# Optimization experiments

Hardware: AMD Instinct MI355X
Metric: run time of the kernel (lower is better)

The kernel has to match this reference:

```python
import jax, jax.numpy as jnp
import numpy as np

N_NODES = 100000
N_EDGES = 3200000
N_PAIRS = 500000
D_IN = 256
D_HID = 256
D_OUT = 2


def setup_inputs() -> dict:
    key = jax.random.key(0)
    ks = jax.random.split(key, 9)
    s1 = 1.0 / np.sqrt(D_IN)
    s2 = 1.0 / np.sqrt(D_HID)
    s3 = 1.0 / np.sqrt(2 * D_HID)
    return {
        "x": jax.random.normal(ks[0], (N_NODES, D_IN), jnp.float32),
        "edge_index": jax.random.randint(ks[1], (2, N_EDGES), 0, N_NODES, jnp.int64 if jax.config.jax_enable_x64 else jnp.int32),
        "index": jax.random.randint(ks[2], (N_PAIRS, 2), 0, N_NODES, jnp.int64 if jax.config.jax_enable_x64 else jnp.int32),
        "W1": jax.random.normal(ks[3], (D_HID, D_IN), jnp.float32) * s1,
        "b1": jnp.zeros((D_HID,), jnp.float32),
        "W2": jax.random.normal(ks[4], (D_HID, D_HID), jnp.float32) * s2,
        "b2": jnp.zeros((D_HID,), jnp.float32),
        "W3": jax.random.normal(ks[5], (D_OUT, 2 * D_HID), jnp.float32) * s3,
        "b3": jnp.zeros((D_OUT,), jnp.float32),
    }


def _gin_conv(x, edge_index, W, b):
    # PyG GINConv (eps=0): nn((1+eps)*x + sum_{j in N(i)} x_j)
    src, dst = edge_index[0], edge_index[1]
    agg = jax.ops.segment_sum(x[src], dst, num_segments=x.shape[0])  # [N, d]
    return (x + agg) @ W.T + b


def reference(x, edge_index, index, W1, b1, W2, b2, W3, b3):
    h = jax.nn.relu(_gin_conv(x, edge_index, W1, b1))   # [N, D_HID]
    h = jax.nn.relu(_gin_conv(h, edge_index, W2, b2))   # [N, D_HID]
    pair = jnp.concatenate((h[index[:, 0]], h[index[:, 1]]), axis=-1)  # [P, 2*D_HID]
    logits = pair @ W3.T + b3                            # [P, D_OUT]
    return jax.nn.log_softmax(logits, axis=1)
```

## Files before the change

### kernel.cpp

```cpp
#include <hip/hip_runtime.h>
#include <hip/hip_bf16.h>

constexpr int N_NODES = 100000;
constexpr int N_EDGES = 3200000;
constexpr int N_PAIRS = 500000;
constexpr int D       = 256;
constexpr int NRANGE  = 8;
constexpr int RSPAN   = 12500;
constexpr int SCANN   = 100352;
constexpr int RCAP    = 410000;

using frag_ab = __attribute__((ext_vector_type(8))) short;
using frag_cd = __attribute__((ext_vector_type(4))) float;
typedef unsigned short ushort8 __attribute__((ext_vector_type(8)));

static __device__ __forceinline__ float b2f(unsigned short u) {
  return __uint_as_float(((unsigned)u) << 16);
}
static __device__ __forceinline__ unsigned short f2bf(float f) {
  unsigned u = __float_as_uint(f);
  unsigned r = (u + 0x7fff + ((u >> 16) & 1)) >> 16;
  return (unsigned short)r;
}

__global__ void conv_all(const float4* __restrict__ x, const float4* __restrict__ W1,
                         const float4* __restrict__ W2, ushort4* __restrict__ xb,
                         ushort4* __restrict__ W1b, ushort4* __restrict__ W2b,
                         int4* __restrict__ counts4, int* __restrict__ rc, int n4x) {
  const int nconv = n4x + 2 * 16384;
  const int total = nconv + SCANN / 4;
  int i = blockIdx.x * blockDim.x + threadIdx.x;
  if (i < NRANGE) rc[i] = i * RCAP;
  const int stride = gridDim.x * blockDim.x;
  for (; i < total; i += stride) {
    if (i < nconv) {
      float4 v; ushort4* dst; int k;
      if (i < n4x) { v = x[i]; dst = xb; k = i; }
      else if (i < n4x + 16384) { k = i - n4x; v = W1[k]; dst = W1b; }
      else { k = i - n4x - 16384; v = W2[k]; dst = W2b; }
      ushort4 o;
      o.x = f2bf(v.x); o.y = f2bf(v.y); o.z = f2bf(v.z); o.w = f2bf(v.w);
      dst[k] = o;
    } else {
      int4 z; z.x = 0; z.y = 0; z.z = 0; z.w = 0;
      counts4[i - nconv] = z;
    }
  }
}

constexpr int PART_SEG = 4096;
__global__ __launch_bounds__(256) void part_hist(const int* __restrict__ ei,
                                                 int* __restrict__ counts,
                                                 int* __restrict__ rc,
                                                 int* __restrict__ bucket) {
  __shared__ int lcnt[NRANGE];
  __shared__ int lbase[NRANGE];
  const int t = threadIdx.x;
  const int base = blockIdx.x * PART_SEG;
  if (t < NRANGE) lcnt[t] = 0;
  __syncthreads();

  int rnk[16], rng[16], pv[16];
#pragma unroll
  for (int j = 0; j < 16; ++j) {
    const int i = base + j * 256 + t;
    if (i < N_EDGES) {
      const int sv = ei[i];
      const int dv = ei[N_EDGES + i];
      atomicAdd(&counts[dv], 1);
      rng[j] = dv / RSPAN;
      pv[j] = sv | ((dv - rng[j] * RSPAN) << 17);
      rnk[j] = atomicAdd(&lcnt[rng[j]], 1);
    } else rng[j] = -1;
  }
  __syncthreads();
  if (t < NRANGE) lbase[t] = atomicAdd(&rc[t], lcnt[t]);
  __syncthreads();
#pragma unroll
  for (int j = 0; j < 16; ++j) {
    if (rng[j] >= 0) bucket[lbase[rng[j]] + rnk[j]] = pv[j];
  }
}

__global__ __launch_bounds__(1024) void scan_block_k(const int* __restrict__ in,
                                                     int* __restrict__ out,
                                                     int* __restrict__ bsum) {
  __shared__ int wsum[16];
  const int t = threadIdx.x, lane = t & 63, w = t >> 6;
  const int gid = blockIdx.x * 1024 + t;
  const int v = in[gid];
  int s = v;
#pragma unroll
  for (int off = 1; off < 64; off <<= 1) {
    int u = __shfl_up(s, off, 64);
    if (lane >= off) s += u;
  }
  if (lane == 63) wsum[w] = s;
  __syncthreads();
  if (t < 16) {
    int ws = wsum[t];
#pragma unroll
    for (int off = 1; off < 16; off <<= 1) {
      int u = __shfl_up(ws, off, 64);
      if (lane >= off) ws += u;
    }
    wsum[t] = ws;
  }
  __syncthreads();
  const int wpre = (w == 0) ? 0 : wsum[w - 1];
  out[gid] = wpre + s - v;
  if (t == 1023) bsum[blockIdx.x] = wsum[15];
}

__global__ __launch_bounds__(1024) void scan_small(const int* __restrict__ in,
                                                   int* __restrict__ out, int n) {
  __shared__ int wsum[16];
  const int t = threadIdx.x, lane = t & 63, w = t >> 6;
  int v = (t < n) ? in[t] : 0;
  int s = v;
#pragma unroll
  for (int off = 1; off < 64; off <<= 1) {
    int u = __shfl_up(s, off, 64);
    if (lane >= off) s += u;
  }
  if (lane == 63) wsum[w] = s;
  __syncthreads();
  if (t < 16) {
    int ws = wsum[t];
#pragma unroll
    for (int off = 1; off < 16; off <<= 1) {
      int u = __shfl_up(ws, off, 64);
      if (lane >= off) ws += u;
    }
    wsum[t] = ws;
  }
  __syncthreads();
  const int wpre = (w == 0) ? 0 : wsum[w - 1];
  if (t < n) out[t] = wpre + s - v;
}

__global__ __launch_bounds__(1024) void scan_add_k(int* __restrict__ cursor,
                                                   int* __restrict__ pos,
                                                   const int* __restrict__ bsum2) {
  const int gid = blockIdx.x * 1024 + threadIdx.x;
  const int v = cursor[gid] + bsum2[gid >> 10];
  cursor[gid] = v;
  pos[gid] = v;
}

constexpr int FLB = 128;
__global__ __launch_bounds__(256) void fill_local(const int* __restrict__ bucket,
                                                  const int* __restrict__ rc,
                                                  int* __restrict__ pos,
                                                  int* __restrict__ csr) {
  const int r = blockIdx.x & 7;
  const int j = blockIdx.x >> 3;
  const int rbase = r * RSPAN;
  const int beg = r * RCAP;
  const int end = rc[r];
  for (int i = beg + j * 256 + threadIdx.x; i < end; i += FLB * 256) {
    const int e = bucket[i];
    const int src = e & 0x1FFFF;
    const int dst = rbase + (e >> 17);
    const int p = atomicAdd(&pos[dst], 1);
    csr[p] = src;
  }
}

__global__ __launch_bounds__(256) void gather_agg_bf16(const ushort* __restrict__ x,
                                                       const int* __restrict__ csr,
                                                       const int* __restrict__ cursor,
                                                       const int* __restrict__ counts,
                                                       ushort* __restrict__ out) {
  const int node = blockIdx.x * 4 + (threadIdx.x >> 6);
  const int lane = threadIdx.x & 63;
  const int half = lane >> 5;
  const int fl   = lane & 31;
  if (node >= N_NODES) return;
  const int beg = cursor[node];
  const int end = beg + counts[node];
  const size_t fo = (size_t)fl * 8;

  float acc[8];
#pragma unroll
  for (int j = 0; j < 8; ++j) acc[j] = 0.f;

  if (half == 0) {
    const ushort8 self = *reinterpret_cast<const ushort8*>(x + (size_t)node * D + fo);
#pragma unroll
    for (int j = 0; j < 8; ++j) acc[j] += b2f(self[j]);
  }

  int o = beg + half;
  for (; o + 6 < end; o += 8) {
    const int s0 = csr[o], s1 = csr[o + 2], s2 = csr[o + 4], s3 = csr[o + 6];
    const ushort8 v0 = *reinterpret_cast<const ushort8*>(x + (size_t)s0 * D + fo);
    const ushort8 v1 = *reinterpret_cast<const ushort8*>(x + (size_t)s1 * D + fo);
    const ushort8 v2 = *reinterpret_cast<const ushort8*>(x + (size_t)s2 * D + fo);
    const ushort8 v3 = *reinterpret_cast<const ushort8*>(x + (size_t)s3 * D + fo);
#pragma unroll
    for (int j = 0; j < 8; ++j)
      acc[j] += (b2f(v0[j]) + b2f(v1[j])) + (b2f(v2[j]) + b2f(v3[j]));
  }
  for (; o < end; o += 2) {
    const ushort8 v = *reinterpret_cast<const ushort8*>(x + (size_t)csr[o] * D + fo);
#pragma unroll
    for (int j = 0; j < 8; ++j) acc[j] += b2f(v[j]);
  }

#pragma unroll
  for (int j = 0; j < 8; ++j) acc[j] += __shfl_xor(acc[j], 32, 64);

  if (half == 0) {
    ushort8 ov;
#pragma unroll
    for (int j = 0; j < 8; ++j) ov[j] = f2bf(acc[j]);
    *reinterpret_cast<ushort8*>(out + (size_t)node * D + fo) = ov;
  }
}

constexpr int GEMM_NWG = ((N_NODES + 63) / 64) * 4;
constexpr int GEMM_Q   = GEMM_NWG / 8;
constexpr int GEMM_R   = GEMM_NWG % 8;
constexpr int CT_PITCH = 72;

template <bool WRITE_C>
__global__ __launch_bounds__(256) void gemm_mfma(const ushort* __restrict__ A,
                                                 const ushort* __restrict__ W,
                                                 const float* __restrict__ bias,
                                                 ushort* __restrict__ C,
                                                 const float* __restrict__ W3,
                                                 float* __restrict__ projp,
                                                 int M) {
  __shared__ __align__(16) ushort As[64 * 256];
  __shared__ __align__(16) ushort Ws[64 * 256];

  const int orig = blockIdx.x;
  const int xcd  = orig & 7;
  const int jj   = orig >> 3;
  const int base_ = (xcd < GEMM_R) ? xcd * (GEMM_Q + 1)
                                   : GEMM_R * (GEMM_Q + 1) + (xcd - GEMM_R) * GEMM_Q;
  const int swz  = base_ + jj;
  const int row0 = (swz >> 2) * 64;
  const int col0 = (swz & 3) * 64;
  const int ct   = swz & 3;

  const int t = threadIdx.x;
  const int w = t >> 6, l = t & 63;

  {
    const float4 zero4 = {0.f, 0.f, 0.f, 0.f};
#pragma unroll
    for (int i = 0; i < 8; ++i) {
      const int chunk = t + i * 256;
      const int r  = chunk >> 5;
      const int kb = (chunk & 31) << 4;
      const int swzb = kb ^ ((r & 7) << 4);
      const int grow = row0 + r;
      float4 av = zero4;
      if (grow < M)
        av = *reinterpret_cast<const float4*>(
            reinterpret_cast<const char*>(A) + (size_t)grow * 512 + kb);
      *reinterpret_cast<float4*>(reinterpret_cast<char*>(As) + r * 512 + swzb) = av;
      const float4 wv = *reinterpret_cast<const float4*>(
          reinterpret_cast<const char*>(W) + (size_t)(col0 + r) * 512 + kb);
      *reinterpret_cast<float4*>(reinterpret_cast<char*>(Ws) + r * 512 + swzb) = wv;
    }
  }
  __syncthreads();

  const int g  = l >> 4;
  const int fr = l & 15;

  frag_cd acc[4];
#pragma unroll
  for (int c = 0; c < 4; ++c) {
    acc[c][0] = 0.f; acc[c][1] = 0.f; acc[c][2] = 0.f; acc[c][3] = 0.f;
  }

  const int arow = w * 16 + fr;
  const char* Asb = reinterpret_cast<const char*>(As);
  const char* Wsb = reinterpret_cast<const char*>(Ws);
#pragma unroll
  for (int ks = 0; ks < 8; ++ks) {
    const int kb = ks * 64 + g * 16;
    const frag_ab af = *reinterpret_cast<const frag_ab*>(
        Asb + arow * 512 + (kb ^ ((arow & 7) << 4)));
#pragma unroll
    for (int c = 0; c < 4; ++c) {
      const int wrow = c * 16 + fr;
      const frag_ab bf = *reinterpret_cast<const frag_ab*>(
          Wsb + wrow * 512 + (kb ^ ((wrow & 7) << 4)));
      acc[c] = __builtin_amdgcn_mfma_f32_16x16x32_bf16(af, bf, acc[c], 0, 0, 0);
    }
  }
  __syncthreads();

  ushort* Ct = As;
#pragma unroll
  for (int c = 0; c < 4; ++c) {
    const int col = c * 16 + fr;
    const float bv = bias[col0 + col];
#pragma unroll
    for (int r = 0; r < 4; ++r) {
      const int rl = w * 16 + g * 4 + r;
      Ct[rl * CT_PITCH + col] = f2bf(fmaxf(acc[c][r] + bv, 0.f));
    }
  }
  __syncthreads();

  if constexpr (WRITE_C) {
#pragma unroll
    for (int i = 0; i < 2; ++i) {
      const int chunk = t + i * 256;
      const int r  = chunk >> 3;
      const int cb = (chunk & 7) << 4;
      const int grow = row0 + r;
      if (grow < M)
        *reinterpret_cast<float4*>(reinterpret_cast<char*>(C) + (size_t)grow * 512 + col0 * 2 + cb) =
            *reinterpret_cast<const float4*>(
                reinterpret_cast<const char*>(Ct) + r * (CT_PITCH * 2) + cb);
    }
  } else {
    const int r = t >> 2;
    const int q = t & 3;
    const int grow = row0 + r;
    float pa0 = 0.f, pa1 = 0.f, pb0 = 0.f, pb1 = 0.f;
    if (grow < M) {
      const ushort8 u8a = *reinterpret_cast<const ushort8*>(&Ct[r * CT_PITCH + q * 16]);
      const ushort8 u8b = *reinterpret_cast<const ushort8*>(&Ct[r * CT_PITCH + q * 16 + 8]);
#pragma unroll
      for (int j = 0; j < 16; ++j) {
        const float hv = b2f(j < 8 ? u8a[j] : u8b[j - 8]);
        const int gc = col0 + q * 16 + j;
        pa0 += hv * W3[gc];
        pa1 += hv * W3[512 + gc];
        pb0 += hv * W3[256 + gc];
        pb1 += hv * W3[768 + gc];
      }
    }
    pa0 += __shfl_xor(pa0, 1, 64); pa0 += __shfl_xor(pa0, 2, 64);
    pa1 += __shfl_xor(pa1, 1, 64); pa1 += __shfl_xor(pa1, 2, 64);
    pb0 += __shfl_xor(pb0, 1, 64); pb0 += __shfl_xor(pb0, 2, 64);
    pb1 += __shfl_xor(pb1, 1, 64); pb1 += __shfl_xor(pb1, 2, 64);
    if (q == 0 && grow < M) {
      float4 o; o.x = pa0; o.y = pa1; o.z = pb0; o.w = pb1;
      *reinterpret_cast<float4*>(&projp[((size_t)ct * N_NODES + grow) * 4]) = o;
    }
  }
}

__global__ __launch_bounds__(256) void proj_reduce(const float4* __restrict__ projp,
                                                   float4* __restrict__ proj) {
  const int node = blockIdx.x * blockDim.x + threadIdx.x;
  if (node >= N_NODES) return;
  float4 s = projp[node];
#pragma unroll
  for (int ct = 1; ct < 4; ++ct) {
    const float4 v = projp[(size_t)ct * N_NODES + node];
    s.x += v.x; s.y += v.y; s.z += v.z; s.w += v.w;
  }
  proj[node] = s;
}

__global__ __launch_bounds__(256) void pair_lite(const float4* __restrict__ proj,
                                                 const int* __restrict__ idx,
                                                 const float* __restrict__ b3,
                                                 float* __restrict__ out) {
  const int p = blockIdx.x * blockDim.x + threadIdx.x;
  if (p >= N_PAIRS) return;
  const int2 ii = reinterpret_cast<const int2*>(idx)[p];
  const float4 pa = proj[ii.x];
  const float4 pb = proj[ii.y];
  float l0 = pa.x + pb.z + b3[0];
  float l1 = pa.y + pb.w + b3[1];
  const float m = fmaxf(l0, l1);
  const float lse = m + logf(expf(l0 - m) + expf(l1 - m));
  float2 o; o.x = l0 - lse; o.y = l1 - lse;
  reinterpret_cast<float2*>(out)[p] = o;
}

extern "C" void kernel_launch(void* const* d_in, const int* in_sizes, int n_in,
                              void* d_out, int out_size, void* d_ws, size_t ws_size,
                              hipStream_t stream) {
  const float* x   = (const float*)d_in[0];
  const int*   ei  = (const int*)d_in[1];
  const int*   idx = (const int*)d_in[2];
  const float* W1  = (const float*)d_in[3];
  const float* b1  = (const float*)d_in[4];
  const float* W2  = (const float*)d_in[5];
  const float* b2  = (const float*)d_in[6];
  const float* W3  = (const float*)d_in[7];
  const float* b3  = (const float*)d_in[8];
  float* out = (float*)d_out;

  char* ws = (char*)d_ws;
  ushort* xb    = (ushort*)(ws);
  ushort* aggb  = (ushort*)(ws + 51200000);
  int*    bucket= (int*)(ws + 51200000);
  ushort* hb    = (ushort*)(ws + 102400000);
  float* projp  = (float*)(ws + 102400000);
  float* projf  = (float*)(ws + 108800000);
  ushort* W1b   = (ushort*)(ws + 153600000);
  ushort* W2b   = (ushort*)(ws + 153731072);
  int* counts   = (int*)(ws + 153862144);
  int* cursor   = (int*)(ws + 154263552);
  int* pos      = (int*)(ws + 154664960);
  int* csr      = (int*)(ws + 155066368);
  int* bsum     = (int*)(ws + 169466368);
  int* bsum2    = (int*)(ws + 169466880);
  int* rc       = (int*)(ws + 169467392);

  const dim3 blk(256);
  const size_t feat = (size_t)N_NODES * D;
  constexpr int SCAN_BLOCKS = SCANN / 1024;
  const dim3 partGrid((N_EDGES + PART_SEG - 1) / PART_SEG);
  const dim3 flocGrid(NRANGE * FLB);
  const dim3 nodeGrid((N_NODES + 3) / 4);
  const dim3 gemmGrid(GEMM_NWG);
  const dim3 nodeThreadGrid((N_NODES + 255) / 256);
  const dim3 pairGrid((N_PAIRS + 255) / 256);

  conv_all<<<dim3(4096), blk, 0, stream>>>((const float4*)x, (const float4*)W1,
                                           (const float4*)W2, (ushort4*)xb,
                                           (ushort4*)W1b, (ushort4*)W2b,
                                           (int4*)counts, rc, (int)(feat / 4));

  part_hist<<<partGrid, blk, 0, stream>>>(ei, counts, rc, bucket);
  scan_block_k<<<dim3(SCAN_BLOCKS), dim3(1024), 0, stream>>>(counts, cursor, bsum);
  scan_small<<<1, 1024, 0, stream>>>(bsum, bsum2, SCAN_BLOCKS);
  scan_add_k<<<dim3(SCAN_BLOCKS), dim3(1024), 0, stream>>>(cursor, pos, bsum2);
  fill_local<<<flocGrid, blk, 0, stream>>>(bucket, rc, pos, csr);

  gather_agg_bf16<<<nodeGrid, blk, 0, stream>>>(xb, csr, cursor, counts, aggb);
  gemm_mfma<true><<<gemmGrid, blk, 0, stream>>>(aggb, W1b, b1, hb, nullptr, nullptr, N_NODES);

  gather_agg_bf16<<<nodeGrid, blk, 0, stream>>>(hb, csr, cursor, counts, aggb);
  gemm_mfma<false><<<gemmGrid, blk, 0, stream>>>(aggb, W2b, b2, nullptr, W3, projp, N_NODES);

  proj_reduce<<<nodeThreadGrid, blk, 0, stream>>>((const float4*)projp, (float4*)projf);
  pair_lite<<<pairGrid, blk, 0, stream>>>((const float4*)projf, idx, b3, out);
}
```

Baseline: 897.1 us.

## Fuse conversion with partitioning, merge scan passes, drop pos array and proj_reduce

Edge partitioning now shares a kernel with the bf16 conversion of features and weights, so the two run concurrently in one launch; zeroing moves to memsets. The three-stage scan becomes two kernels, with each block re-summing the block totals serially. fill_local takes slots by decrementing counts instead of using a separate pos array, and gather reads cursor[node+1] for the end. proj_reduce is folded into the pair kernel, which now reads four partial projections per endpoint. This cuts launches and memory passes, but doubles random gathers in the pair stage and adds a serial loop per scan block.

```diff
diff --git a/kernel.cpp b/kernel.cpp
--- a/kernel.cpp
+++ b/kernel.cpp
@@ -23,17 +23,53 @@
   return (unsigned short)r;
 }
 
-__global__ void conv_all(const float4* __restrict__ x, const float4* __restrict__ W1,
-                         const float4* __restrict__ W2, ushort4* __restrict__ xb,
-                         ushort4* __restrict__ W1b, ushort4* __restrict__ W2b,
-                         int4* __restrict__ counts4, int* __restrict__ rc, int n4x) {
-  const int nconv = n4x + 2 * 16384;
-  const int total = nconv + SCANN / 4;
-  int i = blockIdx.x * blockDim.x + threadIdx.x;
-  if (i < NRANGE) rc[i] = i * RCAP;
-  const int stride = gridDim.x * blockDim.x;
-  for (; i < total; i += stride) {
-    if (i < nconv) {
+constexpr int PART_SEG    = 4096;
+constexpr int PART_BLOCKS = (N_EDGES + PART_SEG - 1) / PART_SEG;
+constexpr int CONV_BLOCKS = 4096;
+
+__global__ __launch_bounds__(256) void conv_part(const int* __restrict__ ei,
+                                                 int* __restrict__ counts,
+                                                 int* __restrict__ rc,
+                                                 int* __restrict__ bucket,
+                                                 const float4* __restrict__ x,
+                                                 const float4* __restrict__ W1,
+                                                 const float4* __restrict__ W2,
+                                                 ushort4* __restrict__ xb,
+                                                 ushort4* __restrict__ W1b,
+                                                 ushort4* __restrict__ W2b, int n4x) {
+  const int t = threadIdx.x;
+  if (blockIdx.x < PART_BLOCKS) {
+    __shared__ int lcnt[NRANGE];
+    __shared__ int lbase[NRANGE];
+    const int base = blockIdx.x * PART_SEG;
+    if (t < NRANGE) lcnt[t] = 0;
+    __syncthreads();
+
+    int rnk[16], rng[16], pv[16];
+#pragma unroll
+    for (int j = 0; j < 16; ++j) {
+      const int i = base + j * 256 + t;
+      if (i < N_EDGES) {
+        const int sv = ei[i];
+        const int dv = ei[N_EDGES + i];
+        atomicAdd(&counts[dv], 1);
+        rng[j] = dv / RSPAN;
+        pv[j] = sv | ((dv - rng[j] * RSPAN) << 17);
+        rnk[j] = atomicAdd(&lcnt[rng[j]], 1);
+      } else rng[j] = -1;
+    }
+    __syncthreads();
+    if (t < NRANGE) lbase[t] = t * RCAP + atomicAdd(&rc[t], lcnt[t]);
+    __syncthreads();
+#pragma unroll
+    for (int j = 0; j < 16; ++j) {
+      if (rng[j] >= 0) bucket[lbase[rng[j]] + rnk[j]] = pv[j];
+    }
+  } else {
+    const int nconv = n4x + 2 * 16384;
+    int i = (blockIdx.x - PART_BLOCKS) * 256 + t;
+    const int stride = CONV_BLOCKS * 256;
+    for (; i < nconv; i += stride) {
       float4 v; ushort4* dst; int k;
       if (i < n4x) { v = x[i]; dst = xb; k = i; }
       else if (i < n4x + 16384) { k = i - n4x; v = W1[k]; dst = W1b; }
@@ -41,44 +77,7 @@
       ushort4 o;
       o.x = f2bf(v.x); o.y = f2bf(v.y); o.z = f2bf(v.z); o.w = f2bf(v.w);
       dst[k] = o;
-    } else {
-      int4 z; z.x = 0; z.y = 0; z.z = 0; z.w = 0;
-      counts4[i - nconv] = z;
-    }
-  }
-}
-
-constexpr int PART_SEG = 4096;
-__global__ __launch_bounds__(256) void part_hist(const int* __restrict__ ei,
-                                                 int* __restrict__ counts,
-                                                 int* __restrict__ rc,
-                                                 int* __restrict__ bucket) {
-  __shared__ int lcnt[NRANGE];
-  __shared__ int lbase[NRANGE];
-  const int t = threadIdx.x;
-  const int base = blockIdx.x * PART_SEG;
-  if (t < NRANGE) lcnt[t] = 0;
-  __syncthreads();
-
-  int rnk[16], rng[16], pv[16];
-#pragma unroll
-  for (int j = 0; j < 16; ++j) {
-    const int i = base + j * 256 + t;
-    if (i < N_EDGES) {
-      const int sv = ei[i];
-      const int dv = ei[N_EDGES + i];
-      atomicAdd(&counts[dv], 1);
-      rng[j] = dv / RSPAN;
-      pv[j] = sv | ((dv - rng[j] * RSPAN) << 17);
-      rnk[j] = atomicAdd(&lcnt[rng[j]], 1);
-    } else rng[j] = -1;
-  }
-  __syncthreads();
-  if (t < NRANGE) lbase[t] = atomicAdd(&rc[t], lcnt[t]);
-  __syncthreads();
-#pragma unroll
-  for (int j = 0; j < 16; ++j) {
-    if (rng[j] >= 0) bucket[lbase[rng[j]] + rnk[j]] = pv[j];
+    }
   }
 }
 
@@ -112,57 +111,40 @@
   if (t == 1023) bsum[blockIdx.x] = wsum[15];
 }
 
-__global__ __launch_bounds__(1024) void scan_small(const int* __restrict__ in,
-                                                   int* __restrict__ out, int n) {
-  __shared__ int wsum[16];
-  const int t = threadIdx.x, lane = t & 63, w = t >> 6;
-  int v = (t < n) ? in[t] : 0;
-  int s = v;
-#pragma unroll
-  for (int off = 1; off < 64; off <<= 1) {
-    int u = __shfl_up(s, off, 64);
-    if (lane >= off) s += u;
-  }
-  if (lane == 63) wsum[w] = s;
-  __syncthreads();
-  if (t < 16) {
-    int ws = wsum[t];
-#pragma unroll
-    for (int off = 1; off < 16; off <<= 1) {
-      int u = __shfl_up(ws, off, 64);
-      if (lane >= off) ws += u;
-    }
-    wsum[t] = ws;
-  }
-  __syncthreads();
-  const int wpre = (w == 0) ? 0 : wsum[w - 1];
-  if (t < n) out[t] = wpre + s - v;
-}
-
-__global__ __launch_bounds__(1024) void scan_add_k(int* __restrict__ cursor,
-                                                   int* __restrict__ pos,
-                                                   const int* __restrict__ bsum2) {
-  const int gid = blockIdx.x * 1024 + threadIdx.x;
-  const int v = cursor[gid] + bsum2[gid >> 10];
-  cursor[gid] = v;
-  pos[gid] = v;
+constexpr int SCAN_BLOCKS = SCANN / 1024;
+__global__ __launch_bounds__(1024) void scan_addf(int* __restrict__ cursor,
+                                                  const int* __restrict__ bsum) {
+  __shared__ int bs[SCAN_BLOCKS];
+  __shared__ int bs2[SCAN_BLOCKS];
+  const int t = threadIdx.x;
+  if (t < SCAN_BLOCKS) bs[t] = bsum[t];
+  __syncthreads();
+  if (t == 0) {
+    int run = 0;
+#pragma unroll 1
+    for (int k = 0; k < SCAN_BLOCKS; ++k) { bs2[k] = run; run += bs[k]; }
+  }
+  __syncthreads();
+  const int gid = blockIdx.x * 1024 + t;
+  cursor[gid] += bs2[blockIdx.x];
 }
 
 constexpr int FLB = 128;
 __global__ __launch_bounds__(256) void fill_local(const int* __restrict__ bucket,
                                                   const int* __restrict__ rc,
-                                                  int* __restrict__ pos,
+                                                  const int* __restrict__ cursor,
+                                                  int* __restrict__ counts,
                                                   int* __restrict__ csr) {
   const int r = blockIdx.x & 7;
   const int j = blockIdx.x >> 3;
   const int rbase = r * RSPAN;
   const int beg = r * RCAP;
-  const int end = rc[r];
+  const int end = beg + rc[r];
   for (int i = beg + j * 256 + threadIdx.x; i < end; i += FLB * 256) {
     const int e = bucket[i];
     const int src = e & 0x1FFFF;
     const int dst = rbase + (e >> 17);
-    const int p = atomicAdd(&pos[dst], 1);
+    const int p = cursor[dst] + atomicSub(&counts[dst], 1) - 1;
     csr[p] = src;
   }
 }
@@ -170,7 +152,6 @@
 __global__ __launch_bounds__(256) void gather_agg_bf16(const ushort* __restrict__ x,
                                                        const int* __restrict__ csr,
                                                        const int* __restrict__ cursor,
-                                                       const int* __restrict__ counts,
                                                        ushort* __restrict__ out) {
   const int node = blockIdx.x * 4 + (threadIdx.x >> 6);
   const int lane = threadIdx.x & 63;
@@ -178,7 +159,7 @@
   const int fl   = lane & 31;
   if (node >= N_NODES) return;
   const int beg = cursor[node];
-  const int end = beg + counts[node];
+  const int end = cursor[node + 1];
   const size_t fo = (size_t)fl * 8;
 
   float acc[8];
@@ -350,30 +331,21 @@
   }
 }
 
-__global__ __launch_bounds__(256) void proj_reduce(const float4* __restrict__ projp,
-                                                   float4* __restrict__ proj) {
-  const int node = blockIdx.x * blockDim.x + threadIdx.x;
-  if (node >= N_NODES) return;
-  float4 s = projp[node];
-#pragma unroll
-  for (int ct = 1; ct < 4; ++ct) {
-    const float4 v = projp[(size_t)ct * N_NODES + node];
-    s.x += v.x; s.y += v.y; s.z += v.z; s.w += v.w;
-  }
-  proj[node] = s;
-}
-
-__global__ __launch_bounds__(256) void pair_lite(const float4* __restrict__ proj,
-                                                 const int* __restrict__ idx,
-                                                 const float* __restrict__ b3,
-                                                 float* __restrict__ out) {
+__global__ __launch_bounds__(256) void pair_fused(const float4* __restrict__ projp,
+                                                  const int* __restrict__ idx,
+                                                  const float* __restrict__ b3,
+                                                  float* __restrict__ out) {
   const int p = blockIdx.x * blockDim.x + threadIdx.x;
   if (p >= N_PAIRS) return;
   const int2 ii = reinterpret_cast<const int2*>(idx)[p];
-  const float4 pa = proj[ii.x];
-  const float4 pb = proj[ii.y];
-  float l0 = pa.x + pb.z + b3[0];
-  float l1 = pa.y + pb.w + b3[1];
+  float l0 = b3[0], l1 = b3[1];
+#pragma unroll
+  for (int ct = 0; ct < 4; ++ct) {
+    const float4 pa = projp[(size_t)ct * N_NODES + ii.x];
+    const float4 pb = projp[(size_t)ct * N_NODES + ii.y];
+    l0 += pa.x + pb.z;
+    l1 += pa.y + pb.w;
+  }
   const float m = fmaxf(l0, l1);
   const float lse = m + logf(expf(l0 - m) + expf(l1 - m));
   float2 o; o.x = l0 - lse; o.y = l1 - lse;
@@ -400,44 +372,39 @@
   int*    bucket= (int*)(ws + 51200000);
   ushort* hb    = (ushort*)(ws + 102400000);
   float* projp  = (float*)(ws + 102400000);
-  float* projf  = (float*)(ws + 108800000);
   ushort* W1b   = (ushort*)(ws + 153600000);
   ushort* W2b   = (ushort*)(ws + 153731072);
   int* counts   = (int*)(ws + 153862144);
   int* cursor   = (int*)(ws + 154263552);
-  int* pos      = (int*)(ws + 154664960);
   int* csr      = (int*)(ws + 155066368);
   int* bsum     = (int*)(ws + 169466368);
-  int* bsum2    = (int*)(ws + 169466880);
   int* rc       = (int*)(ws + 169467392);
 
   const dim3 blk(256);
   const size_t feat = (size_t)N_NODES * D;
-  constexpr int SCAN_BLOCKS = SCANN / 1024;
-  const dim3 partGrid((N_EDGES + PART_SEG - 1) / PART_SEG);
+  const dim3 cpGrid(PART_BLOCKS + CONV_BLOCKS);
   const dim3 flocGrid(NRANGE * FLB);
   const dim3 nodeGrid((N_NODES + 3) / 4);
   const dim3 gemmGrid(GEMM_NWG);
-  const dim3 nodeThreadGrid((N_NODES + 255) / 256);
   const dim3 pairGrid((N_PAIRS + 255) / 256);
 
-  conv_all<<<dim3(4096), blk, 0, stream>>>((const float4*)x, (const float4*)W1,
-                                           (const float4*)W2, (ushort4*)xb,
-                                           (ushort4*)W1b, (ushort4*)W2b,
-                                           (int4*)counts, rc, (int)(feat / 4));
-
-  part_hist<<<partGrid, blk, 0, stream>>>(ei, counts, rc, bucket);
+  hipMemsetAsync(counts, 0, (size_t)SCANN * 4, stream);
+  hipMemsetAsync(rc, 0, NRANGE * 4, stream);
+
+  conv_part<<<cpGrid, blk, 0, stream>>>(ei, counts, rc, bucket,
+                                        (const float4*)x, (const float4*)W1,
+                                        (const float4*)W2, (ushort4*)xb,
+                                        (ushort4*)W1b, (ushort4*)W2b, (int)(feat / 4));
+
   scan_block_k<<<dim3(SCAN_BLOCKS), dim3(1024), 0, stream>>>(counts, cursor, bsum);
-  scan_small<<<1, 1024, 0, stream>>>(bsum, bsum2, SCAN_BLOCKS);
-  scan_add_k<<<dim3(SCAN_BLOCKS), dim3(1024), 0, stream>>>(cursor, pos, bsum2);
-  fill_local<<<flocGrid, blk, 0, stream>>>(bucket, rc, pos, csr);
-
-  gather_agg_bf16<<<nodeGrid, blk, 0, stream>>>(xb, csr, cursor, counts, aggb);
+  scan_addf<<<dim3(SCAN_BLOCKS), dim3(1024), 0, stream>>>(cursor, bsum);
+  fill_local<<<flocGrid, blk, 0, stream>>>(bucket, rc, cursor, counts, csr);
+
+  gather_agg_bf16<<<nodeGrid, blk, 0, stream>>>(xb, csr, cursor, aggb);
   gemm_mfma<true><<<gemmGrid, blk, 0, stream>>>(aggb, W1b, b1, hb, nullptr, nullptr, N_NODES);
 
-  gather_agg_bf16<<<nodeGrid, blk, 0, stream>>>(hb, csr, cursor, counts, aggb);
+  gather_agg_bf16<<<nodeGrid, blk, 0, stream>>>(hb, csr, cursor, aggb);
   gemm_mfma<false><<<gemmGrid, blk, 0, stream>>>(aggb, W2b, b2, nullptr, W3, projp, N_NODES);
 
-  proj_reduce<<<nodeThreadGrid, blk, 0, stream>>>((const float4*)projp, (float4*)projf);
-  pair_lite<<<pairGrid, blk, 0, stream>>>((const float4*)projf, idx, b3, out);
-}
+  pair_fused<<<pairGrid, blk, 0, stream>>>((const float4*)projp, idx, b3, out);
+}
```

After: 918.8 us. +2.4%, slower.
